# Kernel tuning notes

Measured on AMD Instinct MI355X. Metric: run time of the kernel, lower is better.

Reference implementation:

```python
import jax, jax.numpy as jnp
import numpy as np

N_STEPS = 96
BATCH = 16384
N_MAT = 8
N_STRIKES = 8
PERIOD = 12          # N_steps // n_maturities
T_HORIZON = 1.0
RFR = 0.03
S0 = 1.0
LAYER = 128
DT = T_HORIZON / N_STEPS
SQRT_DT = float(np.sqrt(DT))
DF = float(np.exp(-RFR * DT))  # per-step discount factor


def _mlp(Win, bin_, Wh, bh, Wout, bout, x, out_fn):
    # x: [features, batch]; linear layers act on axis 0 (matches torch cat along dim 0)
    h = jax.nn.leaky_relu(Win @ x + bin_[:, None])
    for k in range(Wh.shape[0]):
        h = jax.nn.leaky_relu(Wh[k] @ h + bh[k][:, None])
    return out_fn(Wout @ h + bout[:, None])


def _forward(normals, strikes, lev_Win, lev_bin, lev_Wh, lev_bh, lev_Wout, lev_bout,
             hed_Win, hed_bin, hed_Wh, hed_bh, hed_Wout, hed_bout):
    B = normals.shape[1]
    dt = jnp.float32(DT)
    sqrt_dt = jnp.float32(SQRT_DT)
    r = jnp.float32(RFR)
    df = jnp.float32(DF)
    sg = jax.lax.stop_gradient

    def body(carry, xs):
        S_prev, hedging, prices, variance = carry
        i, nn_i = xs                      # i: int32 step (1..N_STEPS), nn_i: [B] normals
        i_f = i.astype(jnp.float32)
        idx = (i - 1) // PERIOD           # which per-period MLP
        t = ((i_f - 1.0) * dt) * jnp.ones((1, B), jnp.float32)
        X = jnp.concatenate([t, S_prev], axis=0)          # [2, B]
        lev = _mlp(lev_Win[idx], lev_bin[idx], lev_Wh[idx], lev_bh[idx],
                   lev_Wout[idx], lev_bout[idx], X, jax.nn.softplus)  # [1, B]
        drift = S_prev * r / (1.0 + jnp.abs(sg(S_prev) * r) * sqrt_dt)
        diffusion = S_prev * lev / (1.0 + jnp.abs(sg(S_prev * lev)) * sqrt_dt)
        dW = sqrt_dt * nn_i                               # [B]
        S_curr = S_prev + drift * dt + diffusion * dW     # [1, B]
        Xh = jnp.concatenate([t, sg(S_prev)], axis=0)
        hedge = _mlp(hed_Win[idx], hed_bin[idx], hed_Wh[idx], hed_bh[idx],
                     hed_Wout[idx], hed_bout[idx], Xh,
                     lambda y: y).reshape(N_STRIKES, N_MAT, B)
        hedging = hedging + (df ** (i_f - 1.0)) * sg(S_prev * diffusion) * hedge * dW
        # maturity handling (maturities at steps PERIOD, 2*PERIOD, ..., N_STEPS)
        table_idx = jnp.clip(i // PERIOD - 1, 0, N_MAT - 1)
        is_mat = (i % PERIOD == 0).astype(jnp.float32)
        simulated = (df ** i_f) * jnp.maximum(S_curr - strikes[:, None], 0.0) \
                    - hedging[:, table_idx]               # [K, B]
        mean = simulated.mean(axis=1)                     # [K]
        var = jnp.sum((simulated - mean[:, None]) ** 2, axis=1) / (B - 1)  # unbiased, as torch .var()
        prices = prices.at[:, table_idx].add(is_mat * mean)
        variance = variance.at[:, table_idx].add(is_mat * var)
        return (S_curr, hedging, prices, variance), None

    body = jax.checkpoint(body)
    carry0 = (jnp.full((1, B), jnp.float32(S0)),
              jnp.zeros((N_STRIKES, N_MAT, B), jnp.float32),
              jnp.zeros((N_STRIKES, N_MAT), jnp.float32),
              jnp.zeros((N_STRIKES, N_MAT), jnp.float32))
    xs = (jnp.arange(1, N_STEPS + 1, dtype=jnp.int32), normals)
    (_, _, prices, variance), _ = jax.lax.scan(body, carry0, xs)
    return prices, variance


def setup_inputs() -> dict:
    key = jax.random.key(0)
    ks = jax.random.split(key, 16)
    M, L, NH = N_MAT, LAYER, 3  # num_layers=4 -> 3 hidden-to-hidden layers

    def w(k, shape, fan_in):
        return (jax.random.normal(k, shape, jnp.float32) / np.sqrt(fan_in)).astype(jnp.float32)

    inp = {
        "normals": jax.random.normal(ks[0], (N_STEPS, BATCH), jnp.float32),
        "strikes": jnp.linspace(0.8, 1.15, N_STRIKES, dtype=jnp.float32),
        "lev_Win": w(ks[1], (M, L, 2), 2),
        "lev_bin": w(ks[2], (M, L), L),
        "lev_Wh": w(ks[3], (M, NH, L, L), L),
        "lev_bh": w(ks[4], (M, NH, L), L),
        "lev_Wout": w(ks[5], (M, 1, L), L),
        "lev_bout": w(ks[6], (M, 1), L),
        "hed_Win": w(ks[7], (M, L, 2), 2),
        "hed_bin": w(ks[8], (M, L), L),
        "hed_Wh": w(ks[9], (M, NH, L, L), L),
        "hed_bh": w(ks[10], (M, NH, L), L),
        "hed_Wout": w(ks[11], (M, N_STRIKES * N_MAT, L), L),
        "hed_bout": w(ks[12], (M, N_STRIKES * N_MAT), L),
    }
    return inp


def reference(normals, strikes, lev_Win, lev_bin, lev_Wh, lev_bh, lev_Wout, lev_bout,
              hed_Win, hed_bin, hed_Wh, hed_bh, hed_Wout, hed_bout):
    return _forward(normals, strikes, lev_Win, lev_bin, lev_Wh, lev_bh, lev_Wout, lev_bout,
                    hed_Win, hed_bin, hed_Wh, hed_bh, hed_Wout, hed_bout)
```

## Files before the change

### kernel.cpp

```cpp
#include <hip/hip_runtime.h>
#include <math.h>

typedef __attribute__((ext_vector_type(8)))  short  short8;
typedef __attribute__((ext_vector_type(4)))  short  short4v;
typedef __attribute__((ext_vector_type(16))) float  f32x16;
typedef __attribute__((ext_vector_type(4)))  float  f32x4v;

#define DT_F    ((float)(1.0/96.0))
#define SQDT_F  (0.10206207261596575f)
#define DF_F    (0.99968754882437816f)
#define RFR_F   (0.03f)

#define SWZ(c,k) (((c)<<7) + ((k) ^ (((c)&7)<<3)))

static __device__ __forceinline__ short f2bf(float x) {
    return __builtin_bit_cast(short, (__bf16)x);
}
static __device__ __forceinline__ float bf2f(short h) {
    return (float)__builtin_bit_cast(__bf16, h);
}

__device__ __forceinline__ void layer1(const float* __restrict__ Win, const float* __restrict__ bin_,
        float t, const float* __restrict__ sScur, ushort* __restrict__ out, int wvm, int l)
{
    const int g = l >> 4, c15 = l & 15;
    const int r0 = (wvm << 5) + (g << 3);
    float a8[8], w1[8];
#pragma unroll
    for (int jj = 0; jj < 8; ++jj) {
        const int r = r0 + jj;
        a8[jj] = fmaf(Win[2*r], t, bin_[r]);
        w1[jj] = Win[2*r + 1];
    }
#pragma unroll
    for (int cc = 0; cc < 4; ++cc) {
        const int c = c15 + (cc << 4);
        const float S = sScur[c];
        short8 v;
#pragma unroll
        for (int jj = 0; jj < 8; ++jj) {
            float h = fmaf(w1[jj], S, a8[jj]);
            h = fmaxf(h, 0.01f * h);
            v[jj] = f2bf(h);
        }
        *(short8*)&out[SWZ(c, r0)] = v;
    }
}

__device__ __forceinline__ void hidden32(const short8 (&__restrict__ wf)[8], const float* __restrict__ bias,
        const ushort* __restrict__ bin, ushort* __restrict__ bout, int wvm, int l)
{
    const int c0 = l & 31;
    const int l5 = l >> 5;
    const int kr = l5 << 3;
    f32x16 acc0 = {0,0,0,0,0,0,0,0,0,0,0,0,0,0,0,0};
    f32x16 acc1 = acc0;
#pragma unroll
    for (int kc = 0; kc < 8; ++kc) {
        const int k0 = (kc << 4) + kr;
        short8 b0 = *(const short8*)&bin[SWZ(c0,      k0)];
        short8 b1 = *(const short8*)&bin[SWZ(c0 + 32, k0)];
        acc0 = __builtin_amdgcn_mfma_f32_32x32x16_bf16(wf[kc], b0, acc0, 0, 0, 0);
        acc1 = __builtin_amdgcn_mfma_f32_32x32x16_bf16(wf[kc], b1, acc1, 0, 0, 0);
    }
#pragma unroll
    for (int q = 0; q < 4; ++q) {
        const int rloc = (q << 3) + (l5 << 2);
        const f32x4v bq = *(const f32x4v*)&bias[(wvm << 5) + rloc];
        short4v o0, o1;
#pragma unroll
        for (int ii = 0; ii < 4; ++ii) {
            float x0 = acc0[(q << 2) + ii] + bq[ii]; o0[ii] = f2bf(fmaxf(x0, 0.01f * x0));
            float x1 = acc1[(q << 2) + ii] + bq[ii]; o1[ii] = f2bf(fmaxf(x1, 0.01f * x1));
        }
        *(short4v*)&bout[SWZ(c0,      (wvm << 5) + rloc)] = o0;
        *(short4v*)&bout[SWZ(c0 + 32, (wvm << 5) + rloc)] = o1;
    }
}

__global__ __launch_bounds__(512, 2)
void sim_kernel(const float* __restrict__ normals, const float* __restrict__ strikes,
                const float* __restrict__ levWin, const float* __restrict__ levbin,
                const float* __restrict__ levbh,  const float* __restrict__ levWout,
                const float* __restrict__ levbout,
                const float* __restrict__ hedWin, const float* __restrict__ hedbin,
                const float* __restrict__ hedbh,  const float* __restrict__ hedbout,
                const ushort* __restrict__ WF, double* __restrict__ accD)
{
    __shared__ ushort bufL[2][64 * 128];
    __shared__ ushort bufH[2][64 * 128];
    __shared__ float  sS[2][64];
    __shared__ float  sHc[64];

    const int tid  = threadIdx.x;
    const int wv   = tid >> 6;
    const int half = wv >> 2;
    const int wvm  = wv & 3;
    const int l    = tid & 63;
    const int g    = l >> 4;
    const int c15  = l & 15;
    const int bp0  = blockIdx.x * 64;

    if (tid < 64) sS[0][tid] = 1.0f;
    float hedg[4][4];
#pragma unroll
    for (int a = 0; a < 4; ++a)
#pragma unroll
        for (int b = 0; b < 4; ++b) hedg[a][b] = 0.f;
    float dfim1 = 1.0f;

    short8 wCh[3][8];
    short8 wOut[4];
    __syncthreads();

    for (int i = 1; i <= 96; ++i) {
        const int idx = (i - 1) / 12;
        const float t = (float)(i - 1) * DT_F;
        const float* sScur = sS[(i - 1) & 1];
        float* sSnxt = sS[i & 1];
        const ushort* WFi = WF + (size_t)idx * 106496;

        if (((i - 1) % 12) == 0) {
            const ushort* Wm = WFi + ((half * 3) << 14);
#pragma unroll
            for (int m = 0; m < 3; ++m) {
                const short8* fb = (const short8*)(Wm + (m << 14) + (wvm << 12));
#pragma unroll
                for (int kc = 0; kc < 8; ++kc) wCh[m][kc] = fb[kc * 64 + l];
            }
            if (half) {
                const short8* fo = (const short8*)(WFi + 98304 + (wvm << 11));
#pragma unroll
                for (int kcq = 0; kcq < 4; ++kcq) wOut[kcq] = fo[kcq * 64 + l];
            }
        }

        ushort* A = half ? bufH[0] : bufL[0];
        ushort* B = half ? bufH[1] : bufL[1];
        const float* Win  = (half ? hedWin : levWin) + idx * 256;
        const float* binp = (half ? hedbin : levbin) + (idx << 7);
        const float* bh   = (half ? hedbh  : levbh)  + idx * 384;

        layer1(Win, binp, t, sScur, A, wvm, l);
        __syncthreads();
        hidden32(wCh[0], bh,       A, B, wvm, l);
        __syncthreads();
        hidden32(wCh[1], bh + 128, B, A, wvm, l);
        __syncthreads();
        hidden32(wCh[2], bh + 256, A, B, wvm, l);
        __syncthreads();

        const float dfi = dfim1 * DF_F;
        f32x4v acc0 = {0,0,0,0}, acc1 = acc0, acc2 = acc0, acc3 = acc0;
        if (half == 0) {
            const float* Wo = levWout + (idx << 7);
            float wk[32];
#pragma unroll
            for (int kb = 0; kb < 8; ++kb)
                *(f32x4v*)&wk[4 * kb] = *(const f32x4v*)&Wo[(g << 5) + (kb << 2)];
            const int c = c15 + (wvm << 4);
            float p = 0.f;
#pragma unroll
            for (int kb = 0; kb < 4; ++kb) {
                short8 hv = *(const short8*)&bufL[1][SWZ(c, (g << 5) + (kb << 3))];
#pragma unroll
                for (int j = 0; j < 8; ++j) p = fmaf(bf2f(hv[j]), wk[(kb << 3) + j], p);
            }
            p += __shfl_xor(p, 16);
            p += __shfl_xor(p, 32);
            p += levbout[idx];
            const float lv = (p > 20.f) ? p : log1pf(expf(p));
            const float S = sScur[c];
            const float drift = S * RFR_F / (1.f + fabsf(S * RFR_F) * SQDT_F);
            const float dif   = S * lv    / (1.f + fabsf(S * lv)   * SQDT_F);
            const float dW = SQDT_F * normals[(i - 1) * 16384 + bp0 + c];
            const float Sn = S + drift * DT_F + dif * dW;
            if (g == 0) { sSnxt[c] = Sn; sHc[c] = dfim1 * (S * dif) * dW; }
        } else {
            __builtin_amdgcn_s_setprio(1);
#pragma unroll
            for (int kcq = 0; kcq < 4; ++kcq) {
                const int k0 = (kcq << 5) + (g << 3);
                short8 b0 = *(const short8*)&bufH[1][SWZ(c15,      k0)];
                short8 b1 = *(const short8*)&bufH[1][SWZ(16 + c15, k0)];
                short8 b2 = *(const short8*)&bufH[1][SWZ(32 + c15, k0)];
                short8 b3 = *(const short8*)&bufH[1][SWZ(48 + c15, k0)];
                acc0 = __builtin_amdgcn_mfma_f32_16x16x32_bf16(wOut[kcq], b0, acc0, 0, 0, 0);
                acc1 = __builtin_amdgcn_mfma_f32_16x16x32_bf16(wOut[kcq], b1, acc1, 0, 0, 0);
                acc2 = __builtin_amdgcn_mfma_f32_16x16x32_bf16(wOut[kcq], b2, acc2, 0, 0, 0);
                acc3 = __builtin_amdgcn_mfma_f32_16x16x32_bf16(wOut[kcq], b3, acc3, 0, 0, 0);
            }
            __builtin_amdgcn_s_setprio(0);
        }
        __syncthreads();

        if (half == 1) {
            const f32x4v bo4 = *(const f32x4v*)&hedbout[(idx << 6) + (wvm << 4) + (g << 2)];
            const float hc0 = sHc[c15], hc1 = sHc[16 + c15], hc2 = sHc[32 + c15], hc3 = sHc[48 + c15];
#pragma unroll
            for (int ii = 0; ii < 4; ++ii) {
                hedg[0][ii] = fmaf(hc0, acc0[ii] + bo4[ii], hedg[0][ii]);
                hedg[1][ii] = fmaf(hc1, acc1[ii] + bo4[ii], hedg[1][ii]);
                hedg[2][ii] = fmaf(hc2, acc2[ii] + bo4[ii], hedg[2][ii]);
                hedg[3][ii] = fmaf(hc3, acc3[ii] + bo4[ii], hedg[3][ii]);
            }
            if ((i % 12) == 0) {
                const int m = i / 12 - 1;
                const int isel = m & 3;
                const bool active = ((m >> 2) == (g & 1));
                const int ks = (wvm << 1) + (g >> 1);
                float s_ = 0.f, q_ = 0.f;
                if (active) {
                    const float K = strikes[ks];
#pragma unroll
                    for (int ct = 0; ct < 4; ++ct) {
                        const float* hrow = hedg[ct];
                        const float hv = (isel == 0) ? hrow[0] : (isel == 1) ? hrow[1]
                                        : (isel == 2) ? hrow[2] : hrow[3];
                        const float Sn = sSnxt[(ct << 4) + c15];
                        const float sim = dfi * fmaxf(Sn - K, 0.f) - hv;
                        s_ += sim; q_ += sim * sim;
                    }
                }
#pragma unroll
                for (int off = 1; off < 16; off <<= 1) {
                    s_ += __shfl_xor(s_, off);
                    q_ += __shfl_xor(q_, off);
                }
                if (active && c15 == 0) {
                    const int rep = blockIdx.x & 31;
                    atomicAdd(&accD[rep * 128 + ks * 8 + m], (double)s_);
                    atomicAdd(&accD[rep * 128 + 64 + ks * 8 + m], (double)q_);
                }
            }
        }
        dfim1 = dfi;
    }
}

__global__ void prep_kernel(const float* __restrict__ levWh, const float* __restrict__ hedWh,
                            const float* __restrict__ hedWout,
                            ushort* __restrict__ WF, double* __restrict__ accD)
{
    const long long stride = (long long)gridDim.x * blockDim.x;
    const long long t0 = (long long)blockIdx.x * blockDim.x + threadIdx.x;
    for (long long e = t0; e < 851968LL; e += stride) {
        const int idx = (int)(e / 106496);
        const int rem = (int)(e % 106496);
        float val;
        if (rem < 98304) {
            const int m    = rem >> 14;
            const int r2   = rem & 16383;
            const int slot = r2 >> 9;
            const int rb   = slot >> 3;
            const int kc   = slot & 7;
            const int lane = (r2 >> 3) & 63;
            const int j    = r2 & 7;
            const int r = (rb << 5) + (lane & 31);
            const int k = (kc << 4) + ((lane >> 5) << 3) + j;
            const float* src = (m < 3) ? levWh : hedWh;
            const int mm = (m < 3) ? m : m - 3;
            val = src[(((idx * 3 + mm) << 7) + r) * 128 + k];
        } else {
            const int r3   = rem - 98304;
            const int slot = r3 >> 9;
            const int rb   = slot >> 2;
            const int kcq  = slot & 3;
            const int lane = (r3 >> 3) & 63;
            const int j    = r3 & 7;
            const int r = (rb << 4) + (lane & 15);
            const int k = (kcq << 5) + ((lane >> 4) << 3) + j;
            val = hedWout[(idx << 13) + (r << 7) + k];
        }
        WF[e] = (ushort)f2bf(val);
    }
    for (long long e = t0; e < 4096; e += stride) accD[e] = 0.0;
}

__global__ void finalize_kernel(const double* __restrict__ accD, float* __restrict__ out)
{
    const int t = threadIdx.x;
    if (t < 64) {
        double s = 0.0, q = 0.0;
        for (int rep = 0; rep < 32; ++rep) {
            s += accD[rep * 128 + t];
            q += accD[rep * 128 + 64 + t];
        }
        out[t]      = (float)(s / 16384.0);
        out[64 + t] = (float)((q - s * s / 16384.0) / 16383.0);
    }
}

extern "C" void kernel_launch(void* const* d_in, const int* in_sizes, int n_in,
                              void* d_out, int out_size, void* d_ws, size_t ws_size,
                              hipStream_t stream)
{
    const float* normals = (const float*)d_in[0];
    const float* strikes = (const float*)d_in[1];
    const float* levWin  = (const float*)d_in[2];
    const float* levbin  = (const float*)d_in[3];
    const float* levWh   = (const float*)d_in[4];
    const float* levbh   = (const float*)d_in[5];
    const float* levWout = (const float*)d_in[6];
    const float* levbout = (const float*)d_in[7];
    const float* hedWin  = (const float*)d_in[8];
    const float* hedbin  = (const float*)d_in[9];
    const float* hedWh   = (const float*)d_in[10];
    const float* hedbh   = (const float*)d_in[11];
    const float* hedWout = (const float*)d_in[12];
    const float* hedbout = (const float*)d_in[13];

    ushort* WF   = (ushort*)d_ws;
    double* accD = (double*)((char*)d_ws + 1703936);

    prep_kernel<<<1024, 256, 0, stream>>>(levWh, hedWh, hedWout, WF, accD);
    sim_kernel<<<256, 512, 0, stream>>>(normals, strikes,
                                        levWin, levbin, levbh, levWout, levbout,
                                        hedWin, hedbin, hedbh, hedbout,
                                        WF, accD);
    finalize_kernel<<<1, 64, 0, stream>>>(accD, (float*)d_out);
}
```

Before: 580.7 us.

## Stream hidden-layer weight fragments per layer with double buffering instead of register-caching

Previously each wave kept all three hidden-layer weight fragment sets plus the output fragments resident in registers, reloading them every 12 steps. Now each layer's fragments and biases are loaded from global memory every step into two alternating register buffers, with the next layer's load issued before the current layer's MFMAs to hide latency. Biases are folded into the accumulator initialisation, the normals load is hoisted before a barrier, and softplus uses fast __logf/__expf. This cuts register pressure (possibly spills under launch_bounds(512,2)) at the cost of much more repeated global/L2 traffic per step and slightly reduced softplus accuracy.

```diff
diff --git a/kernel.cpp b/kernel.cpp
--- a/kernel.cpp
+++ b/kernel.cpp
@@ -47,14 +47,32 @@
     }
 }
 
-__device__ __forceinline__ void hidden32(const short8 (&__restrict__ wf)[8], const float* __restrict__ bias,
+__device__ __forceinline__ void load_frags(const ushort* __restrict__ Wm, const float* __restrict__ bias,
+        int wvm, int l, int l5, short8 (&__restrict__ wf)[8], f32x4v (&__restrict__ bi)[4])
+{
+    const short8* fb = (const short8*)(Wm + (wvm << 12));
+#pragma unroll
+    for (int kc = 0; kc < 8; ++kc) wf[kc] = fb[kc * 64 + l];
+#pragma unroll
+    for (int q = 0; q < 4; ++q)
+        bi[q] = *(const f32x4v*)&bias[(wvm << 5) + (q << 3) + (l5 << 2)];
+}
+
+__device__ __forceinline__ void hidden_compute(const short8 (&__restrict__ wf)[8],
+        const f32x4v (&__restrict__ bi)[4],
         const ushort* __restrict__ bin, ushort* __restrict__ bout, int wvm, int l)
 {
     const int c0 = l & 31;
     const int l5 = l >> 5;
     const int kr = l5 << 3;
-    f32x16 acc0 = {0,0,0,0,0,0,0,0,0,0,0,0,0,0,0,0};
-    f32x16 acc1 = acc0;
+    f32x16 acc0, acc1;
+#pragma unroll
+    for (int q = 0; q < 4; ++q)
+#pragma unroll
+        for (int ii = 0; ii < 4; ++ii) {
+            acc0[(q << 2) + ii] = bi[q][ii];
+            acc1[(q << 2) + ii] = bi[q][ii];
+        }
 #pragma unroll
     for (int kc = 0; kc < 8; ++kc) {
         const int k0 = (kc << 4) + kr;
@@ -66,12 +84,11 @@
 #pragma unroll
     for (int q = 0; q < 4; ++q) {
         const int rloc = (q << 3) + (l5 << 2);
-        const f32x4v bq = *(const f32x4v*)&bias[(wvm << 5) + rloc];
         short4v o0, o1;
 #pragma unroll
         for (int ii = 0; ii < 4; ++ii) {
-            float x0 = acc0[(q << 2) + ii] + bq[ii]; o0[ii] = f2bf(fmaxf(x0, 0.01f * x0));
-            float x1 = acc1[(q << 2) + ii] + bq[ii]; o1[ii] = f2bf(fmaxf(x1, 0.01f * x1));
+            float x0 = acc0[(q << 2) + ii]; o0[ii] = f2bf(fmaxf(x0, 0.01f * x0));
+            float x1 = acc1[(q << 2) + ii]; o1[ii] = f2bf(fmaxf(x1, 0.01f * x1));
         }
         *(short4v*)&bout[SWZ(c0,      (wvm << 5) + rloc)] = o0;
         *(short4v*)&bout[SWZ(c0 + 32, (wvm << 5) + rloc)] = o1;
@@ -99,6 +116,7 @@
     const int l    = tid & 63;
     const int g    = l >> 4;
     const int c15  = l & 15;
+    const int l5   = l >> 5;
     const int bp0  = blockIdx.x * 64;
 
     if (tid < 64) sS[0][tid] = 1.0f;
@@ -109,8 +127,8 @@
         for (int b = 0; b < 4; ++b) hedg[a][b] = 0.f;
     float dfim1 = 1.0f;
 
-    short8 wCh[3][8];
-    short8 wOut[4];
+    short8 wfA[8], wfB[8];
+    f32x4v biA[4], biB[4];
     __syncthreads();
 
     for (int i = 1; i <= 96; ++i) {
@@ -119,45 +137,46 @@
         const float* sScur = sS[(i - 1) & 1];
         float* sSnxt = sS[i & 1];
         const ushort* WFi = WF + (size_t)idx * 106496;
-
-        if (((i - 1) % 12) == 0) {
-            const ushort* Wm = WFi + ((half * 3) << 14);
-#pragma unroll
-            for (int m = 0; m < 3; ++m) {
-                const short8* fb = (const short8*)(Wm + (m << 14) + (wvm << 12));
-#pragma unroll
-                for (int kc = 0; kc < 8; ++kc) wCh[m][kc] = fb[kc * 64 + l];
-            }
-            if (half) {
-                const short8* fo = (const short8*)(WFi + 98304 + (wvm << 11));
-#pragma unroll
-                for (int kcq = 0; kcq < 4; ++kcq) wOut[kcq] = fo[kcq * 64 + l];
-            }
-        }
-
-        ushort* A = half ? bufH[0] : bufL[0];
-        ushort* B = half ? bufH[1] : bufL[1];
-        const float* Win  = (half ? hedWin : levWin) + idx * 256;
-        const float* binp = (half ? hedbin : levbin) + (idx << 7);
-        const float* bh   = (half ? hedbh  : levbh)  + idx * 384;
-
-        layer1(Win, binp, t, sScur, A, wvm, l);
-        __syncthreads();
-        hidden32(wCh[0], bh,       A, B, wvm, l);
-        __syncthreads();
-        hidden32(wCh[1], bh + 128, B, A, wvm, l);
-        __syncthreads();
-        hidden32(wCh[2], bh + 256, A, B, wvm, l);
-        __syncthreads();
-
-        const float dfi = dfim1 * DF_F;
-        f32x4v acc0 = {0,0,0,0}, acc1 = acc0, acc2 = acc0, acc3 = acc0;
+        const ushort* Wm  = WFi + ((half * 3) << 14);
+        const float* bh   = (half ? hedbh : levbh) + idx * 384;
+        ushort* buf0 = half ? bufH[0] : bufL[0];
+        ushort* buf1 = half ? bufH[1] : bufL[1];
+
+        load_frags(Wm, bh, wvm, l, l5, wfA, biA);
+        layer1((half ? hedWin : levWin) + idx * 256,
+               (half ? hedbin : levbin) + (idx << 7), t, sScur, buf0, wvm, l);
+        float nrm = 0.f;
+        if (half == 0) nrm = normals[(i - 1) * 16384 + bp0 + c15 + (wvm << 4)];
+        __syncthreads();
+
+        load_frags(Wm + 16384, bh + 128, wvm, l, l5, wfB, biB);
+        hidden_compute(wfA, biA, buf0, buf1, wvm, l);
+        __syncthreads();
+
+        load_frags(Wm + 32768, bh + 256, wvm, l, l5, wfA, biA);
+        hidden_compute(wfB, biB, buf1, buf0, wvm, l);
+        __syncthreads();
+
+        float wk[32];
+        short8 wOut[4];
+        f32x4v bo4;
         if (half == 0) {
             const float* Wo = levWout + (idx << 7);
-            float wk[32];
 #pragma unroll
             for (int kb = 0; kb < 8; ++kb)
                 *(f32x4v*)&wk[4 * kb] = *(const f32x4v*)&Wo[(g << 5) + (kb << 2)];
+        } else {
+            const short8* fo = (const short8*)(WFi + 98304 + (wvm << 11));
+#pragma unroll
+            for (int kcq = 0; kcq < 4; ++kcq) wOut[kcq] = fo[kcq * 64 + l];
+            bo4 = *(const f32x4v*)&hedbout[(idx << 6) + (wvm << 4) + (g << 2)];
+        }
+        hidden_compute(wfA, biA, buf0, buf1, wvm, l);
+        __syncthreads();
+
+        const float dfi = dfim1 * DF_F;
+        f32x4v acc0, acc1, acc2, acc3;
+        if (half == 0) {
             const int c = c15 + (wvm << 4);
             float p = 0.f;
 #pragma unroll
@@ -169,14 +188,15 @@
             p += __shfl_xor(p, 16);
             p += __shfl_xor(p, 32);
             p += levbout[idx];
-            const float lv = (p > 20.f) ? p : log1pf(expf(p));
+            const float lv = (p > 20.f) ? p : __logf(1.f + __expf(p));
             const float S = sScur[c];
             const float drift = S * RFR_F / (1.f + fabsf(S * RFR_F) * SQDT_F);
             const float dif   = S * lv    / (1.f + fabsf(S * lv)   * SQDT_F);
-            const float dW = SQDT_F * normals[(i - 1) * 16384 + bp0 + c];
+            const float dW = SQDT_F * nrm;
             const float Sn = S + drift * DT_F + dif * dW;
             if (g == 0) { sSnxt[c] = Sn; sHc[c] = dfim1 * (S * dif) * dW; }
         } else {
+            acc0 = bo4; acc1 = bo4; acc2 = bo4; acc3 = bo4;
             __builtin_amdgcn_s_setprio(1);
 #pragma unroll
             for (int kcq = 0; kcq < 4; ++kcq) {
@@ -195,14 +215,13 @@
         __syncthreads();
 
         if (half == 1) {
-            const f32x4v bo4 = *(const f32x4v*)&hedbout[(idx << 6) + (wvm << 4) + (g << 2)];
             const float hc0 = sHc[c15], hc1 = sHc[16 + c15], hc2 = sHc[32 + c15], hc3 = sHc[48 + c15];
 #pragma unroll
             for (int ii = 0; ii < 4; ++ii) {
-                hedg[0][ii] = fmaf(hc0, acc0[ii] + bo4[ii], hedg[0][ii]);
-                hedg[1][ii] = fmaf(hc1, acc1[ii] + bo4[ii], hedg[1][ii]);
-                hedg[2][ii] = fmaf(hc2, acc2[ii] + bo4[ii], hedg[2][ii]);
-                hedg[3][ii] = fmaf(hc3, acc3[ii] + bo4[ii], hedg[3][ii]);
+                hedg[0][ii] = fmaf(hc0, acc0[ii], hedg[0][ii]);
+                hedg[1][ii] = fmaf(hc1, acc1[ii], hedg[1][ii]);
+                hedg[2][ii] = fmaf(hc2, acc2[ii], hedg[2][ii]);
+                hedg[3][ii] = fmaf(hc3, acc3[ii], hedg[3][ii]);
             }
             if ((i % 12) == 0) {
                 const int m = i / 12 - 1;
```

Result: slower. 633.1 us (+9.0%).
